# Optimization experiments

Measured on AMD Instinct MI355X. Metric: run time of the kernel, lower is better.

The kernel has to match this reference:

```python
import jax, jax.numpy as jnp
import numpy as np

B, N, K, F, S = 128, 116, 4, 72, 8
TOPK = 10
INTRA_T, INTER_T = 0.1, 0.2


def _safe_corr(f):
    # f: [batch, d, m] -> corr [batch, d, d], matching torch _safe_compute_correlation
    c = f - f.mean(axis=2, keepdims=True)
    cov = jnp.einsum('bim,bjm->bij', c, c)
    var = jnp.diagonal(cov, axis1=1, axis2=2)
    std = jnp.sqrt(jnp.clip(var, 1e-8, None))[:, :, None]
    corr = cov / (std * std.transpose(0, 2, 1) + 1e-8)
    return jnp.clip(corr, -1.0, 1.0)


def _sym(m):
    return (m + m.swapaxes(-1, -2)) * 0.5


def setup_inputs():
    key = jax.random.key(0)
    ks = jax.random.split(key, 8)
    def lin(k, out_d, in_d):
        return jax.random.normal(k, (out_d, in_d), jnp.float32) * (1.0 / np.sqrt(in_d))
    return {
        'band_features': jax.random.normal(ks[0], (B, N, K, F), jnp.float32),
        'attn_weights': jax.random.uniform(ks[1], (B, N, S, K), jnp.float32),
        'intra_thresh_adj': jnp.zeros((), jnp.float32),
        'inter_thresh_adj': jnp.zeros((), jnp.float32),
        'attn_fuse_weight': jnp.asarray(0.5, jnp.float32),
        'intra_W1': lin(ks[2], 64, N), 'intra_b1': jnp.zeros((64,), jnp.float32),
        'intra_W2': lin(ks[3], N, 64), 'intra_b2': jnp.zeros((N,), jnp.float32),
        'inter_W1': lin(ks[4], 32, K), 'inter_b1': jnp.zeros((32,), jnp.float32),
        'inter_W2': lin(ks[5], K, 32), 'inter_b2': jnp.zeros((K,), jnp.float32),
        'comp_W': lin(ks[6], 128, 2 * F + 6), 'comp_b': jnp.zeros((128,), jnp.float32),
    }


def reference(band_features, attn_weights, intra_thresh_adj, inter_thresh_adj,
              attn_fuse_weight, intra_W1, intra_b1, intra_W2, intra_b2,
              inter_W1, inter_b1, inter_W2, inter_b2, comp_W, comp_b):
    dt = band_features.dtype
    # ---- intra-band graph: [B*K, N, N] correlations ----
    x = band_features.transpose(0, 2, 1, 3).reshape(B * K, N, F)
    corr = _safe_corr(x)
    th = INTRA_T + jax.nn.sigmoid(intra_thresh_adj) * 0.2
    tmask = (jnp.abs(corr) > th).astype(dt)
    _, idx = jax.lax.top_k(jnp.abs(corr), min(TOPK, N))  # [B*K, N, k]
    bix = jnp.arange(B * K)[:, None, None]
    rix = jnp.arange(N)[None, :, None]
    kmask = jnp.zeros_like(corr).at[bix, rix, idx].set(1.0)
    sc = jax.nn.relu(_sym(corr * tmask * kmask))
    h = jax.nn.relu(sc.reshape(-1, N) @ intra_W1.T + intra_b1)  # dropout = eval identity
    intra = jax.nn.sigmoid(h @ intra_W2.T + intra_b2).reshape(B * K, N, N)
    intra_adj = _sym(intra).reshape(B, K, N, N)
    # ---- inter-band graph: [B*N, K, K] correlations ----
    y = band_features.reshape(B * N, K, F)
    base = _safe_corr(y)
    a = attn_weights.reshape(B * N, S, K).transpose(0, 2, 1)  # [B*N, K, S]
    acorr = _safe_corr(a)
    fw = jax.nn.sigmoid(attn_fuse_weight)
    base = fw * base + (1.0 - fw) * acorr
    th2 = INTER_T + jax.nn.sigmoid(inter_thresh_adj) * 0.2
    sc2 = jax.nn.relu(_sym(base * (jnp.abs(base) > th2).astype(dt)))
    h2 = jax.nn.relu(sc2.reshape(-1, K) @ inter_W1.T + inter_b1)
    inter = jax.nn.sigmoid(h2 @ inter_W2.T + inter_b2).reshape(B * N, K, K)
    inter_adj = _sym(inter).reshape(B, N, K, K)
    # ---- unified graph assembly (vectorized replacement of nested loops) ----
    kk = jnp.arange(K)
    bd = jnp.zeros((B, K, N, K, N), dt).at[:, kk, :, kk, :].set(
        intra_adj.transpose(1, 0, 2, 3))  # block-diagonal intra blocks
    unified = bd.reshape(B, K * N, K * N)
    kk1, kk2, nn = np.meshgrid(np.arange(K), np.arange(K), np.arange(N), indexing='ij')
    sel = (kk1 != kk2).ravel()
    k1f, k2f, nf = kk1.ravel()[sel], kk2.ravel()[sel], nn.ravel()[sel]
    vals = inter_adj[:, nf, k1f, k2f]  # [B, M]
    unified_adj = unified.at[:, k1f * N + nf, k2f * N + nf].set(vals)
    # ---- node features ----
    node_features = band_features.transpose(0, 2, 1, 3).reshape(B, K * N, F)
    # ---- graph-level features ----
    node_mean = band_features.mean(axis=(1, 2))
    node_std = jnp.std(band_features, axis=(1, 2), ddof=1)  # torch unbiased std
    deg = (intra_adj > 0).astype(dt).sum(axis=3)  # [B, K, N]
    tri = jnp.einsum('bkij,bkji->bki', intra_adj, intra_adj)  # diag of A@A
    clus = tri / (deg ** 2 + 1e-8)
    dens = (inter_adj > 0).astype(dt).mean(axis=(2, 3))  # [B, N]
    stren = inter_adj.mean(axis=(2, 3))
    gf = jnp.concatenate([
        node_mean, node_std,
        deg.mean(axis=(1, 2))[:, None], jnp.std(deg, axis=(1, 2), ddof=1)[:, None],
        clus.mean(axis=(1, 2))[:, None], jnp.std(clus, axis=(1, 2), ddof=1)[:, None],
        dens.mean(axis=1)[:, None], stren.mean(axis=1)[:, None]], axis=1)
    graph_features = jax.nn.relu(gf @ comp_W.T + comp_b)
    # ---- sparsity scalars ----
    intra_sp = 1.0 - (intra_adj > 0).astype(dt).mean()
    inter_sp = 1.0 - (inter_adj > 0).astype(dt).mean()
    it, jt = float(B * K * N * N), float(B * N * K * K)
    total_sp = (intra_sp * it + inter_sp * jt) / (it + jt)
    return (unified_adj, node_features, graph_features, intra_adj, inter_adj,
            intra_sp, inter_sp, total_sp)
```

## Files before the change

kernel.cpp:

```cpp
#include <hip/hip_runtime.h>
#include <math.h>

#define NB 128
#define NN_ 116
#define NK 4
#define NF 72
#define NS 8
#define TOPK 10

#define BK (NB*NK)
#define BN (NB*NN_)
#define NN2 (NN_*NN_)
#define KN (NK*NN_)
#define ROWS (BK*NN_)
#define LROW 117

#define OFF_UNI 0
#define SZ_UNI (NB*KN*KN)
#define OFF_NF (OFF_UNI + SZ_UNI)
#define SZ_NF (NB*KN*NF)
#define OFF_GF (OFF_NF + SZ_NF)
#define SZ_GF (NB*128)
#define OFF_IA (OFF_GF + SZ_GF)
#define SZ_IA (NB*NK*NN_*NN_)
#define OFF_IE (OFF_IA + SZ_IA)
#define SZ_IE (NB*NN_*NK*NK)
#define OFF_SP (OFF_IE + SZ_IE)

#define SCR_SC 0
#define SCR_CORR (SCR_SC + SZ_IA)
#define SCR_DEG (SCR_CORR + SZ_IA)
#define SCR_CLUS (SCR_DEG + ROWS)
#define SCR_DENS (SCR_CLUS + ROWS)
#define SCR_STREN (SCR_DENS + BN)
#define SCR_AUX (SCR_STREN + BN)

#define NFQ (SZ_NF/4)
#define UNQ (SZ_UNI/4)
#define NB_CORR 512
#define NB_INTER (BN/64)
#define NB_COPY 1044

__device__ __forceinline__ float sigmoidf_(float x){ return 1.0f/(1.0f+expf(-x)); }
__device__ __forceinline__ float dot4_(float4 a, float4 b){
    return fmaf(a.x,b.x, fmaf(a.y,b.y, fmaf(a.z,b.z, a.w*b.w)));
}
#define CLIP1(x) fminf(1.0f, fmaxf(-1.0f, (x)))

__global__ __launch_bounds__(256, 1) void k_corr_inter(const float* __restrict__ band,
    const float* __restrict__ attn, const float* __restrict__ thadj2,
    const float* __restrict__ fwp,
    const float* __restrict__ eW1, const float* __restrict__ eb1,
    const float* __restrict__ eW2, const float* __restrict__ eb2,
    float* __restrict__ corr_out, float* __restrict__ inter_out,
    float* __restrict__ dens_out, float* __restrict__ stren_out,
    float* __restrict__ nf)
{
    __shared__ float sx[NF*120];
    __shared__ float smu[120], srs[120];
    __shared__ float sW1[128], sb1[32], sW2[128], sb2[4];
    __shared__ float sMat[256*4];
    int t = threadIdx.x;
    if (blockIdx.x < NB_CORR){
        int bk = blockIdx.x;
        int b = bk >> 2, k = bk & 3;
        const float* xin = band + ((size_t)b*NN_*NK + k)*NF;
        for (int e = t; e < NN_*NF; e += 256){
            int n = e / NF, f = e - n*NF;
            sx[f*120 + n] = xin[(size_t)n*NK*NF + f];
        }
        for (int e = t; e < NF*4; e += 256)
            sx[(e>>2)*120 + NN_ + (e&3)] = 0.0f;
        __syncthreads();
        if (t < NN_){
            float s = 0.f, ss = 0.f;
            for (int f = 0; f < NF; ++f){ float v = sx[f*120+t]; s += v; ss += v*v; }
            float mu = s * (1.0f/NF);
            float sd = sqrtf(fmaxf(ss - s*mu, 1e-8f));
            smu[t] = mu; srs[t] = 1.0f/sd;
        }
        __syncthreads();
        for (int e = t; e < NF*NN_; e += 256){
            int f = e / NN_, n = e - f*NN_;
            sx[f*120+n] = (sx[f*120+n] - smu[n]) * srs[n];
        }
        __syncthreads();
        float* dst = corr_out + (size_t)bk * NN2;
        if (t < 225){
            int ti = t / 15, tj = t - ti*15;
            int i0 = ti*8, j0 = tj*8;
            float acc[8][8] = {};
            for (int f = 0; f < NF; ++f){
                const float4 a0 = *(const float4*)&sx[f*120 + i0];
                const float4 a1 = *(const float4*)&sx[f*120 + i0 + 4];
                const float4 c0 = *(const float4*)&sx[f*120 + j0];
                const float4 c1 = *(const float4*)&sx[f*120 + j0 + 4];
                float av[8] = {a0.x,a0.y,a0.z,a0.w,a1.x,a1.y,a1.z,a1.w};
                float cv[8] = {c0.x,c0.y,c0.z,c0.w,c1.x,c1.y,c1.z,c1.w};
                #pragma unroll
                for (int r = 0; r < 8; ++r)
                    #pragma unroll
                    for (int c = 0; c < 8; ++c)
                        acc[r][c] = fmaf(av[r], cv[c], acc[r][c]);
            }
            #pragma unroll
            for (int r = 0; r < 8; ++r){
                int i = i0 + r;
                if (i < NN_){
                    float4 v0;
                    v0.x = CLIP1(acc[r][0]); v0.y = CLIP1(acc[r][1]);
                    v0.z = CLIP1(acc[r][2]); v0.w = CLIP1(acc[r][3]);
                    *(float4*)&dst[i*NN_ + j0] = v0;
                    if (j0 + 4 <= 112){
                        float4 v1;
                        v1.x = CLIP1(acc[r][4]); v1.y = CLIP1(acc[r][5]);
                        v1.z = CLIP1(acc[r][6]); v1.w = CLIP1(acc[r][7]);
                        *(float4*)&dst[i*NN_ + j0 + 4] = v1;
                    }
                }
            }
        }
    } else if (blockIdx.x < NB_CORR + NB_INTER){
        if (t < 128) sW1[t] = eW1[t];
        if (t < 32) sb1[t] = eb1[t];
        if (t >= 128 && t < 256) sW2[t-128] = eW2[t-128];
        if (t < 4) sb2[t] = eb2[t];
        __syncthreads();
        int l = t & 3;
        int il = t >> 2;
        size_t item = (size_t)(blockIdx.x - NB_CORR)*64 + il;

        const float* xr = band + item*(NK*NF) + l*NF;
        float s=0,p0=0,p1=0,p2=0,p3=0;
        for (int f = 0; f < NF; ++f){
            float v = xr[f];
            float v1=__shfl_xor(v,1), v2=__shfl_xor(v,2), v3=__shfl_xor(v,3);
            s += v; p0=fmaf(v,v,p0); p1=fmaf(v,v1,p1); p2=fmaf(v,v2,p2); p3=fmaf(v,v3,p3);
        }
        float mu = s*(1.0f/NF);
        float mu1=__shfl_xor(mu,1), mu2=__shfl_xor(mu,2), mu3=__shfl_xor(mu,3);
        float sd = sqrtf(fmaxf(p0 - s*mu, 1e-8f));
        float sd1=__shfl_xor(sd,1), sd2=__shfl_xor(sd,2), sd3=__shfl_xor(sd,3);
        float c0 = CLIP1((p0 - (float)NF*mu*mu )/(sd*sd +1e-8f));
        float c1 = CLIP1((p1 - (float)NF*mu*mu1)/(sd*sd1+1e-8f));
        float c2 = CLIP1((p2 - (float)NF*mu*mu2)/(sd*sd2+1e-8f));
        float c3 = CLIP1((p3 - (float)NF*mu*mu3)/(sd*sd3+1e-8f));

        const float* ar = attn + item*(NS*NK) + l;
        float as=0,q0=0,q1=0,q2=0,q3=0;
        #pragma unroll
        for (int s8 = 0; s8 < NS; ++s8){
            float v = ar[s8*NK];
            float v1=__shfl_xor(v,1), v2=__shfl_xor(v,2), v3=__shfl_xor(v,3);
            as += v; q0=fmaf(v,v,q0); q1=fmaf(v,v1,q1); q2=fmaf(v,v2,q2); q3=fmaf(v,v3,q3);
        }
        float am = as*(1.0f/NS);
        float am1=__shfl_xor(am,1), am2=__shfl_xor(am,2), am3=__shfl_xor(am,3);
        float ad = sqrtf(fmaxf(q0 - as*am, 1e-8f));
        float ad1=__shfl_xor(ad,1), ad2=__shfl_xor(ad,2), ad3=__shfl_xor(ad,3);
        float a0 = CLIP1((q0 - (float)NS*am*am )/(ad*ad +1e-8f));
        float a1 = CLIP1((q1 - (float)NS*am*am1)/(ad*ad1+1e-8f));
        float a2 = CLIP1((q2 - (float)NS*am*am2)/(ad*ad2+1e-8f));
        float a3 = CLIP1((q3 - (float)NS*am*am3)/(ad*ad3+1e-8f));

        float fwv = sigmoidf_(fwp[0]);
        float g0 = fwv*c0 + (1.0f-fwv)*a0;
        float g1 = fwv*c1 + (1.0f-fwv)*a1;
        float g2 = fwv*c2 + (1.0f-fwv)*a2;
        float g3 = fwv*c3 + (1.0f-fwv)*a3;
        float th2 = 0.2f + sigmoidf_(thadj2[0])*0.2f;
        float m0 = (fabsf(g0)>th2)?g0:0.f;
        float m1 = (fabsf(g1)>th2)?g1:0.f;
        float m2 = (fabsf(g2)>th2)?g2:0.f;
        float m3 = (fabsf(g3)>th2)?g3:0.f;

        sMat[il*16 + l*4 + (l^0)] = m0;
        sMat[il*16 + l*4 + (l^1)] = m1;
        sMat[il*16 + l*4 + (l^2)] = m2;
        sMat[il*16 + l*4 + (l^3)] = m3;
        __syncthreads();
        float x0 = fmaxf(0.5f*(sMat[il*16 + l*4 + 0] + sMat[il*16 + 0*4 + l]), 0.f);
        float x1 = fmaxf(0.5f*(sMat[il*16 + l*4 + 1] + sMat[il*16 + 1*4 + l]), 0.f);
        float x2 = fmaxf(0.5f*(sMat[il*16 + l*4 + 2] + sMat[il*16 + 2*4 + l]), 0.f);
        float x3 = fmaxf(0.5f*(sMat[il*16 + l*4 + 3] + sMat[il*16 + 3*4 + l]), 0.f);

        float h[32];
        #pragma unroll
        for (int o = 0; o < 32; ++o){
            float acc = sb1[o];
            acc = fmaf(sW1[o*4+0], x0, acc);
            acc = fmaf(sW1[o*4+1], x1, acc);
            acc = fmaf(sW1[o*4+2], x2, acc);
            acc = fmaf(sW1[o*4+3], x3, acc);
            h[o] = fmaxf(acc, 0.f);
        }
        float o0=sb2[0], o1=sb2[1], o2=sb2[2], o3=sb2[3];
        #pragma unroll
        for (int o = 0; o < 32; ++o){
            float hv = h[o];
            o0 = fmaf(sW2[0*32+o], hv, o0);
            o1 = fmaf(sW2[1*32+o], hv, o1);
            o2 = fmaf(sW2[2*32+o], hv, o2);
            o3 = fmaf(sW2[3*32+o], hv, o3);
        }
        o0 = sigmoidf_(o0); o1 = sigmoidf_(o1); o2 = sigmoidf_(o2); o3 = sigmoidf_(o3);
        __syncthreads();
        sMat[il*16 + l*4 + 0] = o0;
        sMat[il*16 + l*4 + 1] = o1;
        sMat[il*16 + l*4 + 2] = o2;
        sMat[il*16 + l*4 + 3] = o3;
        __syncthreads();
        float y0 = 0.5f*(o0 + sMat[il*16 + 0*4 + l]);
        float y1 = 0.5f*(o1 + sMat[il*16 + 1*4 + l]);
        float y2 = 0.5f*(o2 + sMat[il*16 + 2*4 + l]);
        float y3 = 0.5f*(o3 + sMat[il*16 + 3*4 + l]);
        *(float4*)&inter_out[item*16 + l*4] = make_float4(y0,y1,y2,y3);

        float cnt = ((y0>0.f)?1.f:0.f) + ((y1>0.f)?1.f:0.f) + ((y2>0.f)?1.f:0.f) + ((y3>0.f)?1.f:0.f);
        float sum = y0+y1+y2+y3;
        cnt += __shfl_xor(cnt,1); cnt += __shfl_xor(cnt,2);
        sum += __shfl_xor(sum,1); sum += __shfl_xor(sum,2);
        if (l == 0){
            dens_out[item]  = cnt * (1.0f/16.0f);
            stren_out[item] = sum * (1.0f/16.0f);
        }
    } else {
        int gid = (blockIdx.x - NB_CORR - NB_INTER)*256 + t;
        int gsz = NB_COPY*256;
        for (int q = gid; q < NFQ; q += gsz){
            int fq = q % 18;
            int rest = q / 18;
            int b = rest / KN;
            int p = rest - b*KN;
            int k = p / NN_;
            int n = p - k*NN_;
            float4 v = *(const float4*)&band[(((size_t)b*NN_ + n)*NK + k)*NF + fq*4];
            *(float4*)&nf[(size_t)q*4] = v;
        }
    }
}

__global__ __launch_bounds__(512) void k_topk_mask(const float* __restrict__ corr_in,
    const float* __restrict__ thadj, float* __restrict__ sc_out)
{
    __shared__ float sc_[NN_*LROW];
    __shared__ unsigned skm[NN_*4];
    __shared__ unsigned stop[464*10];
    int bk = blockIdx.x;
    int t = threadIdx.x;
    const float* src = corr_in + (size_t)bk*NN2;
    for (int e = t; e < NN2; e += 512){
        int i = e / NN_, j = e - i*NN_;
        sc_[i*LROW + j] = src[e];
    }
    __syncthreads();
    if (t < NN_*4){
        int r = t >> 2, q = t & 3;
        const float* row = &sc_[r*LROW + q*29];
        int jbase = q*29;
        unsigned tv[TOPK];
        #pragma unroll
        for (int p = 0; p < TOPK; ++p) tv[p] = 0u;
        for (int jj = 0; jj < 29; ++jj){
            float c = fabsf(row[jj]);
            unsigned u = (__float_as_uint(c) & 0xFFFFFF80u) | (unsigned)(127 - (jbase + jj));
            #pragma unroll
            for (int p = 0; p < TOPK; ++p){
                unsigned old = tv[p];
                bool gt = u > old;
                tv[p] = gt ? u : old;
                u = gt ? old : u;
            }
        }
        #pragma unroll
        for (int p = 0; p < TOPK; ++p) stop[t*10 + p] = tv[p];
    }
    __syncthreads();
    if (t < NN_){
        const unsigned* L0 = &stop[(4*t+0)*10];
        const unsigned* L1 = &stop[(4*t+1)*10];
        const unsigned* L2 = &stop[(4*t+2)*10];
        const unsigned* L3 = &stop[(4*t+3)*10];
        int i0=0, i1=0, i2=0, i3=0;
        unsigned m0=0,m1=0,m2=0,m3=0;
        #pragma unroll
        for (int p = 0; p < TOPK; ++p){
            unsigned u0 = L0[i0], u1 = L1[i1], u2 = L2[i2], u3 = L3[i3];
            unsigned ua = u0 > u1 ? u0 : u1;
            unsigned ub = u2 > u3 ? u2 : u3;
            unsigned u  = ua > ub ? ua : ub;
            if (u == u0) ++i0; else if (u == u1) ++i1; else if (u == u2) ++i2; else ++i3;
            int j = 127 - (int)(u & 127u);
            unsigned bit = 1u << (j & 31);
            int w = j >> 5;
            if (w == 0) m0 |= bit; else if (w == 1) m1 |= bit; else if (w == 2) m2 |= bit; else m3 |= bit;
        }
        skm[t*4+0]=m0; skm[t*4+1]=m1; skm[t*4+2]=m2; skm[t*4+3]=m3;
    }
    __syncthreads();
    float th = 0.1f + sigmoidf_(thadj[0]) * 0.2f;
    float* dst = sc_out + (size_t)bk * NN2;
    for (int e = t; e < NN2; e += 512){
        int i = e / NN_, j = e - i*NN_;
        float cij = sc_[i*LROW + j];
        float cji = sc_[j*LROW + i];
        bool kij = (skm[i*4 + (j>>5)] >> (j&31)) & 1u;
        bool kji = (skm[j*4 + (i>>5)] >> (i&31)) & 1u;
        float mij = (fabsf(cij) > th && kij) ? cij : 0.0f;
        float mji = (fabsf(cji) > th && kji) ? cji : 0.0f;
        dst[e] = fmaxf(0.5f*(mij+mji), 0.0f);
    }
}

__global__ __launch_bounds__(256) void k_mlp(const float* __restrict__ sc,
    const float* __restrict__ W1, const float* __restrict__ b1,
    const float* __restrict__ W2, const float* __restrict__ b2,
    float* __restrict__ intra)
{
    __shared__ float sA_[14848];
    __shared__ float sH[64*68];
    __shared__ float sb1[64];
    __shared__ float sb2[128];
    int t = threadIdx.x;
    int r0 = blockIdx.x * 64;
    float* srow = sA_;
    float* sW1  = sA_ + 7424;
    for (int e4 = t; e4 < 1856; e4 += 256){
        *(float4*)&srow[e4*4] = *(const float4*)&sc[(size_t)r0*116 + e4*4];
        *(float4*)&sW1[e4*4]  = *(const float4*)&W1[e4*4];
    }
    if (t < 64) sb1[t] = b1[t];
    if (t < 128) sb2[t] = (t < NN_) ? b2[t] : 0.0f;
    __syncthreads();
    {
        int rg = t >> 4, og = t & 15;
        float acc[4][4] = {};
        for (int j4 = 0; j4 < 29; ++j4){
            float4 s[4], w[4];
            #pragma unroll
            for (int m = 0; m < 4; ++m) s[m] = *(const float4*)&srow[(rg+16*m)*116 + j4*4];
            #pragma unroll
            for (int n = 0; n < 4; ++n) w[n] = *(const float4*)&sW1[(og+16*n)*116 + j4*4];
            #pragma unroll
            for (int m = 0; m < 4; ++m)
                #pragma unroll
                for (int n = 0; n < 4; ++n)
                    acc[m][n] += dot4_(s[m], w[n]);
        }
        #pragma unroll
        for (int m = 0; m < 4; ++m)
            #pragma unroll
            for (int n = 0; n < 4; ++n)
                sH[(rg+16*m)*68 + og+16*n] = fmaxf(acc[m][n] + sb1[og+16*n], 0.0f);
    }
    __syncthreads();
    float* sW2 = sA_;
    for (int e = t; e < 128*64; e += 256){
        int j = e >> 6, o = e & 63;
        sW2[j*76 + o] = (j < NN_) ? W2[e] : 0.0f;
    }
    __syncthreads();
    {
        int rg = t >> 4, jg = t & 15;
        float acc[4][8] = {};
        for (int o4 = 0; o4 < 16; ++o4){
            float4 h[4], w[8];
            #pragma unroll
            for (int m = 0; m < 4; ++m) h[m] = *(const float4*)&sH[(rg+16*m)*68 + o4*4];
            #pragma unroll
            for (int q = 0; q < 8; ++q) w[q] = *(const float4*)&sW2[(jg+16*q)*76 + o4*4];
            #pragma unroll
            for (int m = 0; m < 4; ++m)
                #pragma unroll
                for (int q = 0; q < 8; ++q)
                    acc[m][q] += dot4_(h[m], w[q]);
        }
        #pragma unroll
        for (int m = 0; m < 4; ++m){
            int row = r0 + rg + 16*m;
            #pragma unroll
            for (int q = 0; q < 8; ++q){
                int j = jg + 16*q;
                if (j < NN_)
                    intra[(size_t)row*116 + j] = sigmoidf_(acc[m][q] + sb2[j]);
            }
        }
    }
}

__global__ __launch_bounds__(512) void k_sym_intra(const float* __restrict__ intra,
    float* __restrict__ intra_adj, float* __restrict__ deg_out, float* __restrict__ clus_out)
{
    __shared__ float sm[NN_*LROW];
    int bk = blockIdx.x, t = threadIdx.x;
    const float* src = intra + (size_t)bk*NN2;
    for (int e = t; e < NN2; e += 512){
        int i = e / NN_, j = e - i*NN_;
        sm[i*LROW + j] = src[e];
    }
    __syncthreads();
    float* dst = intra_adj + (size_t)bk*NN2;
    for (int e = t; e < NN2; e += 512){
        int i = e / NN_, j = e - i*NN_;
        dst[e] = 0.5f*(sm[i*LROW + j] + sm[j*LROW + i]);
    }
    if (t < NN_*4){
        int r = t >> 2, q = t & 3;
        float tri = 0.f, dg = 0.f;
        for (int jj = 0; jj < 29; ++jj){
            int j = q*29 + jj;
            float v = 0.5f*(sm[r*LROW+j] + sm[j*LROW+r]);
            tri = fmaf(v, v, tri);
            dg += (v > 0.f) ? 1.f : 0.f;
        }
        tri += __shfl_xor(tri,1); tri += __shfl_xor(tri,2);
        dg  += __shfl_xor(dg,1);  dg  += __shfl_xor(dg,2);
        if (q == 0){
            deg_out[(size_t)bk*NN_ + r]  = dg;
            clus_out[(size_t)bk*NN_ + r] = tri / (dg*dg + 1e-8f);
        }
    }
}

__global__ __launch_bounds__(256) void k_gstats_lin(const float* __restrict__ band,
    const float* __restrict__ deg, const float* __restrict__ clus,
    const float* __restrict__ dens, const float* __restrict__ stren,
    const float* __restrict__ Wc, const float* __restrict__ bc,
    float* __restrict__ gfo, float* __restrict__ aux)
{
    int b = blockIdx.x, t = threadIdx.x;
    __shared__ float sGf[152];
    __shared__ float sPs[18*14*4];
    __shared__ float sPq[18*14*4];
    __shared__ float sA[4], sB[4];

    if (t < 252){
        int fq = t % 18, g = t / 18;
        float4 s = make_float4(0,0,0,0), q = make_float4(0,0,0,0);
        const float* base = band + (size_t)b*(KN*NF);
        for (int nk = g; nk < KN; nk += 14){
            float4 v = *(const float4*)&base[nk*NF + fq*4];
            s.x += v.x; s.y += v.y; s.z += v.z; s.w += v.w;
            q.x = fmaf(v.x,v.x,q.x); q.y = fmaf(v.y,v.y,q.y);
            q.z = fmaf(v.z,v.z,q.z); q.w = fmaf(v.w,v.w,q.w);
        }
        int idx = (fq*14 + g)*4;
        *(float4*)&sPs[idx] = s;
        *(float4*)&sPq[idx] = q;
    }
    __syncthreads();
    if (t < NF){
        int fq = t >> 2, e = t & 3;
        float S = 0.f, Q = 0.f;
        for (int g = 0; g < 14; ++g){ S += sPs[(fq*14+g)*4+e]; Q += sPq[(fq*14+g)*4+e]; }
        float mean = S * (1.0f/(float)KN);
        float var = fmaxf((Q - S*mean)/((float)KN - 1.0f), 0.0f);
        sGf[t] = mean;
        sGf[NF + t] = sqrtf(var);
    }
    __syncthreads();

    float s = 0.f, ss = 0.f;
    for (int e = t; e < KN; e += 256){ float v = deg[(size_t)b*KN + e]; s += v; ss += v*v; }
    #pragma unroll
    for (int d = 1; d < 64; d <<= 1){ s += __shfl_xor(s,d); ss += __shfl_xor(ss,d); }
    if ((t & 63) == 0){ sA[t>>6] = s; sB[t>>6] = ss; }
    __syncthreads();
    if (t == 0){
        float S0 = sA[0]+sA[1]+sA[2]+sA[3], S1 = sB[0]+sB[1]+sB[2]+sB[3];
        float Mv = (float)KN, mean = S0/Mv;
        float var = fmaxf((S1 - S0*mean)/(Mv - 1.0f), 0.0f);
        sGf[144] = mean; sGf[145] = sqrtf(var);
        aux[b] = S0;
    }
    __syncthreads();

    s = 0.f; ss = 0.f;
    for (int e = t; e < KN; e += 256){ float v = clus[(size_t)b*KN + e]; s += v; ss += v*v; }
    #pragma unroll
    for (int d = 1; d < 64; d <<= 1){ s += __shfl_xor(s,d); ss += __shfl_xor(ss,d); }
    if ((t & 63) == 0){ sA[t>>6] = s; sB[t>>6] = ss; }
    __syncthreads();
    if (t == 0){
        float S0 = sA[0]+sA[1]+sA[2]+sA[3], S1 = sB[0]+sB[1]+sB[2]+sB[3];
        float Mv = (float)KN, mean = S0/Mv;
        float var = fmaxf((S1 - S0*mean)/(Mv - 1.0f), 0.0f);
        sGf[146] = mean; sGf[147] = sqrtf(var);
    }
    __syncthreads();

    s = 0.f; ss = 0.f;
    for (int e = t; e < NN_; e += 256){ s += dens[(size_t)b*NN_ + e]; ss += stren[(size_t)b*NN_ + e]; }
    #pragma unroll
    for (int d = 1; d < 64; d <<= 1){ s += __shfl_xor(s,d); ss += __shfl_xor(ss,d); }
    if ((t & 63) == 0){ sA[t>>6] = s; sB[t>>6] = ss; }
    __syncthreads();
    if (t == 0){
        float S0 = sA[0]+sA[1]+sA[2]+sA[3], S1 = sB[0]+sB[1]+sB[2]+sB[3];
        sGf[148] = S0 / (float)NN_;
        sGf[149] = S1 / (float)NN_;
        aux[128 + b] = S0 * 16.0f;
    }
    __syncthreads();

    if (t < 128){
        float acc = bc[t];
        const float* w = Wc + (size_t)t*150;
        for (int c = 0; c < 150; ++c) acc = fmaf(sGf[c], w[c], acc);
        gfo[(size_t)b*128 + t] = fmaxf(acc, 0.f);
    }
}

__global__ __launch_bounds__(64) void k_sparsity(const float* __restrict__ aux, float* __restrict__ out3)
{
    int t = threadIdx.x;
    float a = aux[t] + aux[64 + t];
    float c = aux[128 + t] + aux[192 + t];
    #pragma unroll
    for (int d = 1; d < 64; d <<= 1){ a += __shfl_xor(a,d); c += __shfl_xor(c,d); }
    if (t == 0){
        const float it = 6889472.0f, jt = 237568.0f;
        float isp = 1.0f - a/it;
        float jsp = 1.0f - c/jt;
        out3[0] = isp; out3[1] = jsp;
        out3[2] = (isp*it + jsp*jt)/(it + jt);
    }
}

__global__ __launch_bounds__(256) void k_uninf(const float* __restrict__ intra_adj,
    const float* __restrict__ inter_adj, const float* __restrict__ aux,
    float* __restrict__ uni, float* __restrict__ sp, int do_sp)
{
    if (do_sp && blockIdx.x == 0 && threadIdx.x < 64){
        int t = threadIdx.x;
        float a = aux[t] + aux[64 + t];
        float c = aux[128 + t] + aux[192 + t];
        #pragma unroll
        for (int d = 1; d < 64; d <<= 1){ a += __shfl_xor(a,d); c += __shfl_xor(c,d); }
        if (t == 0){
            const float it = 6889472.0f, jt = 237568.0f;
            float isp = 1.0f - a/it;
            float jsp = 1.0f - c/jt;
            sp[0] = isp; sp[1] = jsp;
            sp[2] = (isp*it + jsp*jt)/(it + jt);
        }
    }
    int gid = blockIdx.x*256 + threadIdx.x;
    int gsz = gridDim.x*256;
    for (int q = gid; q < UNQ; q += gsz){
        int row = q / 116;
        int cq  = q - row*116;
        int b = row / KN;
        int p = row - b*KN;
        int k1 = p / NN_;
        int i  = p - k1*NN_;
        int k2 = cq / 29;
        int j0 = cq*4 - k2*NN_;
        float4 v;
        if (k2 == k1){
            v = *(const float4*)&intra_adj[(((size_t)b*NK + k1)*NN_ + i)*NN_ + j0];
        } else {
            int d = i - j0;
            float val = 0.f;
            if (d >= 0 && d < 4)
                val = inter_adj[(((size_t)b*NN_ + i)*NK + k1)*NK + k2];
            v.x = (d==0)?val:0.f;
            v.y = (d==1)?val:0.f;
            v.z = (d==2)?val:0.f;
            v.w = (d==3)?val:0.f;
        }
        *(float4*)&uni[(size_t)q*4] = v;
    }
}

extern "C" void kernel_launch(void* const* d_in, const int* in_sizes, int n_in,
                              void* d_out, int out_size, void* d_ws, size_t ws_size,
                              hipStream_t stream)
{
    const float* band = (const float*)d_in[0];
    const float* attn = (const float*)d_in[1];
    const float* thA  = (const float*)d_in[2];
    const float* thE  = (const float*)d_in[3];
    const float* fw   = (const float*)d_in[4];
    const float* iW1  = (const float*)d_in[5];
    const float* ib1  = (const float*)d_in[6];
    const float* iW2  = (const float*)d_in[7];
    const float* ib2  = (const float*)d_in[8];
    const float* eW1  = (const float*)d_in[9];
    const float* eb1  = (const float*)d_in[10];
    const float* eW2  = (const float*)d_in[11];
    const float* eb2  = (const float*)d_in[12];
    const float* cW   = (const float*)d_in[13];
    const float* cb   = (const float*)d_in[14];

    float* out = (float*)d_out;
    float* uni = out + OFF_UNI;
    float* nf  = out + OFF_NF;
    float* gfo = out + OFF_GF;
    float* ia  = out + OFF_IA;
    float* ie  = out + OFF_IE;
    float* sp  = out + OFF_SP;

    float* scr_sc    = uni + SCR_SC;
    float* scr_corr  = uni + SCR_CORR;
    float* scr_deg   = uni + SCR_DEG;
    float* scr_clus  = uni + SCR_CLUS;
    float* scr_dens  = uni + SCR_DENS;
    float* scr_stren = uni + SCR_STREN;

    int ws_ok = (ws_size >= 256*sizeof(float));
    float* aux = ws_ok ? (float*)d_ws : (uni + SCR_AUX);

    k_corr_inter<<<NB_CORR + NB_INTER + NB_COPY, 256, 0, stream>>>(
        band, attn, thE, fw, eW1, eb1, eW2, eb2,
        scr_corr, ie, scr_dens, scr_stren, nf);
    k_topk_mask<<<BK, 512, 0, stream>>>(scr_corr, thA, scr_sc);
    k_mlp<<<ROWS/64, 256, 0, stream>>>(scr_sc, iW1, ib1, iW2, ib2, scr_sc);
    k_sym_intra<<<BK, 512, 0, stream>>>(scr_sc, ia, scr_deg, scr_clus);
    k_gstats_lin<<<NB, 256, 0, stream>>>(band, scr_deg, scr_clus, scr_dens, scr_stren,
                                         cW, cb, gfo, aux);
    if (!ws_ok)
        k_sparsity<<<1, 64, 0, stream>>>(aux, sp);
    k_uninf<<<2048, 256, 0, stream>>>(ia, ie, aux, uni, sp, ws_ok ? 1 : 0);
}
```

Before: 153.1 us.

## Fuse intra-band MLP with symmetrization and degree/clustering stats per graph

Merges the row-tiled MLP kernel and the symmetrize/degree kernel into one kernel with one block per (batch, band) graph. The sigmoid MLP output stays in shared memory and is symmetrized there, so the intermediate NxN matrix no longer makes a global write and re-read, and one launch is removed. In exchange, each block uses about 127 KB of shared memory, so fewer blocks fit per CU, the grid shrinks from about 928 to 512 blocks, and 48 of the 512 threads sit idle during the GEMMs. A no-op arithmetic rewrite of the total sparsity expression is also included.

```diff
diff --git a/kernel.cpp b/kernel.cpp
--- a/kernel.cpp
+++ b/kernel.cpp
@@ -312,35 +312,37 @@
     }
 }
 
-__global__ __launch_bounds__(256) void k_mlp(const float* __restrict__ sc,
+__global__ __launch_bounds__(512) void k_mlpsym(const float* __restrict__ sc,
     const float* __restrict__ W1, const float* __restrict__ b1,
     const float* __restrict__ W2, const float* __restrict__ b2,
-    float* __restrict__ intra)
+    float* __restrict__ ia, float* __restrict__ deg_out, float* __restrict__ clus_out)
 {
-    __shared__ float sA_[14848];
-    __shared__ float sH[64*68];
-    __shared__ float sb1[64];
-    __shared__ float sb2[128];
-    int t = threadIdx.x;
-    int r0 = blockIdx.x * 64;
-    float* srow = sA_;
-    float* sW1  = sA_ + 7424;
-    for (int e4 = t; e4 < 1856; e4 += 256){
-        *(float4*)&srow[e4*4] = *(const float4*)&sc[(size_t)r0*116 + e4*4];
-        *(float4*)&sW1[e4*4]  = *(const float4*)&W1[e4*4];
-    }
+    __shared__ float smem[31844];
+    float* sA  = smem;
+    float* sB  = smem + 14036;
+    float* sH  = smem + 23764;
+    float* sb1 = smem + 31652;
+    float* sb2 = smem + 31716;
+    int bk = blockIdx.x, t = threadIdx.x;
+
+    const float* src = sc + (size_t)bk*NN2;
+    for (int e4 = t; e4 < NN2/4; e4 += 512)
+        *(float4*)&sA[e4*4] = *(const float4*)&src[e4*4];
+    for (int e4 = t; e4 < 1856; e4 += 512)
+        *(float4*)&sB[e4*4] = *(const float4*)&W1[e4*4];
     if (t < 64) sb1[t] = b1[t];
-    if (t < 128) sb2[t] = (t < NN_) ? b2[t] : 0.0f;
-    __syncthreads();
-    {
+    if (t >= 64 && t < 192) sb2[t-64] = (t-64 < NN_) ? b2[t-64] : 0.0f;
+    __syncthreads();
+
+    if (t < 464){
         int rg = t >> 4, og = t & 15;
         float acc[4][4] = {};
         for (int j4 = 0; j4 < 29; ++j4){
             float4 s[4], w[4];
             #pragma unroll
-            for (int m = 0; m < 4; ++m) s[m] = *(const float4*)&srow[(rg+16*m)*116 + j4*4];
-            #pragma unroll
-            for (int n = 0; n < 4; ++n) w[n] = *(const float4*)&sW1[(og+16*n)*116 + j4*4];
+            for (int m = 0; m < 4; ++m) s[m] = *(const float4*)&sA[(rg+29*m)*116 + j4*4];
+            #pragma unroll
+            for (int n = 0; n < 4; ++n) w[n] = *(const float4*)&sB[(og+16*n)*116 + j4*4];
             #pragma unroll
             for (int m = 0; m < 4; ++m)
                 #pragma unroll
@@ -351,24 +353,25 @@
         for (int m = 0; m < 4; ++m)
             #pragma unroll
             for (int n = 0; n < 4; ++n)
-                sH[(rg+16*m)*68 + og+16*n] = fmaxf(acc[m][n] + sb1[og+16*n], 0.0f);
-    }
-    __syncthreads();
-    float* sW2 = sA_;
-    for (int e = t; e < 128*64; e += 256){
+                sH[(rg+29*m)*68 + og+16*n] = fmaxf(acc[m][n] + sb1[og+16*n], 0.0f);
+    }
+    __syncthreads();
+
+    for (int e = t; e < 128*64; e += 512){
         int j = e >> 6, o = e & 63;
-        sW2[j*76 + o] = (j < NN_) ? W2[e] : 0.0f;
-    }
-    __syncthreads();
-    {
+        sB[j*76 + o] = (j < NN_) ? W2[e] : 0.0f;
+    }
+    __syncthreads();
+
+    if (t < 464){
         int rg = t >> 4, jg = t & 15;
         float acc[4][8] = {};
         for (int o4 = 0; o4 < 16; ++o4){
             float4 h[4], w[8];
             #pragma unroll
-            for (int m = 0; m < 4; ++m) h[m] = *(const float4*)&sH[(rg+16*m)*68 + o4*4];
-            #pragma unroll
-            for (int q = 0; q < 8; ++q) w[q] = *(const float4*)&sW2[(jg+16*q)*76 + o4*4];
+            for (int m = 0; m < 4; ++m) h[m] = *(const float4*)&sH[(rg+29*m)*68 + o4*4];
+            #pragma unroll
+            for (int q = 0; q < 8; ++q) w[q] = *(const float4*)&sB[(jg+16*q)*76 + o4*4];
             #pragma unroll
             for (int m = 0; m < 4; ++m)
                 #pragma unroll
@@ -377,39 +380,34 @@
         }
         #pragma unroll
         for (int m = 0; m < 4; ++m){
-            int row = r0 + rg + 16*m;
+            int row = rg + 29*m;
             #pragma unroll
             for (int q = 0; q < 8; ++q){
                 int j = jg + 16*q;
                 if (j < NN_)
-                    intra[(size_t)row*116 + j] = sigmoidf_(acc[m][q] + sb2[j]);
+                    sA[row*121 + j] = sigmoidf_(acc[m][q] + sb2[j]);
             }
         }
     }
-}
-
-__global__ __launch_bounds__(512) void k_sym_intra(const float* __restrict__ intra,
-    float* __restrict__ intra_adj, float* __restrict__ deg_out, float* __restrict__ clus_out)
-{
-    __shared__ float sm[NN_*LROW];
-    int bk = blockIdx.x, t = threadIdx.x;
-    const float* src = intra + (size_t)bk*NN2;
-    for (int e = t; e < NN2; e += 512){
-        int i = e / NN_, j = e - i*NN_;
-        sm[i*LROW + j] = src[e];
-    }
-    __syncthreads();
-    float* dst = intra_adj + (size_t)bk*NN2;
-    for (int e = t; e < NN2; e += 512){
-        int i = e / NN_, j = e - i*NN_;
-        dst[e] = 0.5f*(sm[i*LROW + j] + sm[j*LROW + i]);
-    }
-    if (t < NN_*4){
+    __syncthreads();
+
+    float* dia = ia + (size_t)bk*NN2;
+    for (int e4 = t; e4 < NN2/4; e4 += 512){
+        int e = e4*4;
+        int i = e / NN_, j0 = e - i*NN_;
+        float4 v;
+        v.x = 0.5f*(sA[i*121+j0+0] + sA[(j0+0)*121+i]);
+        v.y = 0.5f*(sA[i*121+j0+1] + sA[(j0+1)*121+i]);
+        v.z = 0.5f*(sA[i*121+j0+2] + sA[(j0+2)*121+i]);
+        v.w = 0.5f*(sA[i*121+j0+3] + sA[(j0+3)*121+i]);
+        *(float4*)&dia[e] = v;
+    }
+    if (t < 464){
         int r = t >> 2, q = t & 3;
         float tri = 0.f, dg = 0.f;
         for (int jj = 0; jj < 29; ++jj){
             int j = q*29 + jj;
-            float v = 0.5f*(sm[r*LROW+j] + sm[j*LROW+r]);
+            float v = 0.5f*(sA[r*121+j] + sA[j*121+r]);
             tri = fmaf(v, v, tri);
             dg += (v > 0.f) ? 1.f : 0.f;
         }
@@ -542,7 +540,8 @@
             float isp = 1.0f - a/it;
             float jsp = 1.0f - c/jt;
             sp[0] = isp; sp[1] = jsp;
-            sp[2] = (isp*it + jsp*jt)/(it + jt);
+            sp[2] = (isp*it + jt*0.0f + jsp*jt - jsp*jt + jsp*jt)/(it + jt) * 0.0f
+                    + (isp*it + jsp*jt)/(it + jt);
         }
     }
     int gid = blockIdx.x*256 + threadIdx.x;
@@ -615,8 +614,7 @@
         band, attn, thE, fw, eW1, eb1, eW2, eb2,
         scr_corr, ie, scr_dens, scr_stren, nf);
     k_topk_mask<<<BK, 512, 0, stream>>>(scr_corr, thA, scr_sc);
-    k_mlp<<<ROWS/64, 256, 0, stream>>>(scr_sc, iW1, ib1, iW2, ib2, scr_sc);
-    k_sym_intra<<<BK, 512, 0, stream>>>(scr_sc, ia, scr_deg, scr_clus);
+    k_mlpsym<<<BK, 512, 0, stream>>>(scr_sc, iW1, ib1, iW2, ib2, ia, scr_deg, scr_clus);
     k_gstats_lin<<<NB, 256, 0, stream>>>(band, scr_deg, scr_clus, scr_dens, scr_stren,
                                          cW, cb, gfo, aux);
     if (!ws_ok)
```

Measured after the change: 149.7 us. 1.02x faster.
